# Kernel tuning notes

Hardware: AMD Instinct MI355X
Metric: run time of the kernel (lower is better)

Reference implementation:

```python
import jax, jax.numpy as jnp
import numpy as np
from jax import lax

HW = 256 * 256      # patch h*w
WINDOW = 65536
STRIDE = 32768


def _conv2d(x, w, b, stride, pad):
    y = lax.conv_general_dilated(x, w, (stride, stride), [(pad, pad), (pad, pad)],
                                 dimension_numbers=('NCHW', 'OIHW', 'NCHW'))
    return y + b[None, :, None, None]


def _fcn(x, w1, b1, w2, b2, w3, b3, w4, b4):
    x = jax.nn.relu(_conv2d(x, w1, b1, 6, 6))
    x = jax.nn.relu(_conv2d(x, w2, b2, 4, 4))
    x = jax.nn.relu(_conv2d(x, w3, b3, 2, 2))
    x = jax.nn.relu(_conv2d(x, w4, b4, 1, 1))
    return x


def _avgpool2(x):
    # torch AvgPool2d(2,2,padding=1), count_include_pad=True -> sum window / 4
    s = lax.reduce_window(x, 0.0, lax.add, (1, 1, 2, 2), (1, 1, 2, 2),
                          [(0, 0), (0, 0), (1, 1), (1, 1)])
    return s * 0.25


def _cca(x, qw, qb, kw, kb, vw, vb, gamma):
    B, C, H, W = x.shape
    q = _conv2d(x, qw, qb, 1, 0)   # (B, C//8, H, W)
    k = _conv2d(x, kw, kb, 1, 0)
    v = _conv2d(x, vw, vb, 1, 0)   # (B, C, H, W)
    # column (height-axis) energies with -inf on the diagonal (self position)
    eH = jnp.einsum('bchw,bcgw->bhwg', q, k)                     # (B,H,W,H')
    eH = jnp.where(jnp.eye(H, dtype=bool)[:, None, :], -jnp.inf, eH)
    # row (width-axis) energies
    eW = jnp.einsum('bchw,bchv->bhwv', q, k)                     # (B,H,W,W')
    att = jax.nn.softmax(jnp.concatenate([eH, eW], axis=3), axis=3)
    outH = jnp.einsum('bcgw,bhwg->bchw', v, att[..., :H])
    outW = jnp.einsum('bchv,bhwv->bchw', v, att[..., H:])
    return gamma * (outH + outW) + x


def _forward(x, f0_w1, f0_b1, f0_w2, f0_b2, f0_w3, f0_b3, f0_w4, f0_b4,
             f1_w1, f1_b1, f1_w2, f1_b2, f1_w3, f1_b3, f1_w4, f1_b4,
             qw, qb, kw, kb, vw, vb, gamma, cls_w, cls_b):
    B, nc, L = x.shape
    need = HW - L % HW                 # torch pads a full extra block when L % hw == 0
    xp = jnp.pad(x, ((0, 0), (0, 0), (0, need)))
    nw = (L + need - WINDOW) // STRIDE + 1
    idx = jnp.arange(nw)[:, None] * STRIDE + jnp.arange(WINDOW)[None, :]
    wins = xp[:, 0, :][:, idx]                      # (B, nw, WINDOW) ~ torch unfold
    # torch does a raw reshape (nw,1,h,w) -> (1,1,h*w,nw); row-major reshape matches
    c_in = wins.reshape(B, 1, HW, nw)
    c0 = _fcn(c_in, f0_w1, f0_b1, f0_w2, f0_b2, f0_w3, f0_b3, f0_w4, f0_b4)
    c1 = _fcn(_avgpool2(c_in), f1_w1, f1_b1, f1_w2, f1_b2, f1_w3, f1_b3, f1_w4, f1_b4)
    a0 = _cca(c0, qw, qb, kw, kb, vw, vb, gamma)
    a1 = _cca(c1, qw, qb, kw, kb, vw, vb, gamma)   # 'twoheadfcn' reuses cca_attn0
    feat = jnp.concatenate([a0.mean(axis=(2, 3)), a1.mean(axis=(2, 3))], axis=1)
    return feat @ cls_w.T + cls_b                   # dropout = identity at eval


def setup_inputs():
    key = jax.random.key(0)
    ks = jax.random.split(key, 32)

    def he(k, shape):
        fan_in = int(np.prod(shape[1:]))
        return (jax.random.normal(k, shape) / np.sqrt(fan_in)).astype(jnp.float32)

    inp = {'x': jax.random.uniform(ks[0], (2, 1, 4194304), dtype=jnp.float32)}
    shapes = [(64, 1, 12, 12), (128, 64, 8, 8), (256, 128, 5, 5), (128, 256, 3, 3)]
    for pre, off in (('f0', 1), ('f1', 9)):
        for i, s in enumerate(shapes):
            inp[f'{pre}_w{i+1}'] = he(ks[off + 2 * i], s)
            inp[f'{pre}_b{i+1}'] = (0.01 * jax.random.normal(ks[off + 2 * i + 1], (s[0],))).astype(jnp.float32)
    inp['qw'] = he(ks[17], (16, 128, 1, 1)); inp['qb'] = jnp.zeros((16,), jnp.float32)
    inp['kw'] = he(ks[18], (16, 128, 1, 1)); inp['kb'] = jnp.zeros((16,), jnp.float32)
    inp['vw'] = he(ks[19], (128, 128, 1, 1)); inp['vb'] = jnp.zeros((128,), jnp.float32)
    inp['gamma'] = jnp.full((1,), 0.1, jnp.float32)
    inp['cls_w'] = he(ks[20], (2, 256)); inp['cls_b'] = jnp.zeros((2,), jnp.float32)
    return inp


def reference(x, f0_w1, f0_b1, f0_w2, f0_b2, f0_w3, f0_b3, f0_w4, f0_b4,
              f1_w1, f1_b1, f1_w2, f1_b2, f1_w3, f1_b3, f1_w4, f1_b4,
              qw, qb, kw, kb, vw, vb, gamma, cls_w, cls_b):
    return _forward(x, f0_w1, f0_b1, f0_w2, f0_b2, f0_w3, f0_b3, f0_w4, f0_b4,
                    f1_w1, f1_b1, f1_w2, f1_b2, f1_w3, f1_b3, f1_w4, f1_b4,
                    qw, qb, kw, kb, vw, vb, gamma, cls_w, cls_b)
```

## Files before the change

kernel.cpp:

```cpp
#include <hip/hip_runtime.h>
#include <math.h>

#define BLK 256
static const long LX = 4194304;

typedef __bf16 bf16x8 __attribute__((ext_vector_type(8)));
typedef float  f32x4  __attribute__((ext_vector_type(4)));
typedef unsigned short u16;

__device__ __forceinline__ void bf16split(float x, u16& h, u16& l) {
    unsigned u = __float_as_uint(x);
    unsigned hr = (u + 0x7fffu + ((u >> 16) & 1u)) >> 16;
    h = (u16)hr;
    float hf = __uint_as_float(hr << 16);
    float r = x - hf;
    unsigned v = __float_as_uint(r);
    unsigned lr2 = (v + 0x7fffu + ((v >> 16) & 1u)) >> 16;
    l = (u16)lr2;
}

__device__ __forceinline__ float cin_val(const float* __restrict__ x, long xbase, int h, int w) {
    if ((unsigned)h >= 65536u || (unsigned)w >= 129u) return 0.f;
    long flat = (long)h * 129 + w;
    int n = (int)(flat >> 16);
    int q = (int)(flat & 65535);
    long pos = (long)n * 32768 + q;
    return (pos < LX) ? x[xbase + pos] : 0.f;
}

__global__ __launch_bounds__(256)
void conv1_mfma_k(const float* __restrict__ x, const u16* __restrict__ wbh,
                  const u16* __restrict__ wbl, const float* __restrict__ bias,
                  u16* __restrict__ outh, u16* __restrict__ outl) {
    const long SPT = 240306;
    __shared__ u16 ph[6400];
    __shared__ u16 pl[6400];
    const int tid = threadIdx.x;
    const int b = blockIdx.y;
    const long sp0 = (long)blockIdx.x * 128;
    const long xbase = (long)b * LX;
    const int ho_min = (int)sp0 / 22;
    const int flat_start = (ho_min * 6 - 6) * 129 - 6;
    for (int i = tid; i < 6400; i += 256) {
        int flat = flat_start + i;
        float v = 0.f;
        if (flat >= 0 && flat < 65536 * 129) {
            int n = flat >> 16, q = flat & 65535;
            long pos = (long)n * 32768 + q;
            if (pos < LX) v = x[xbase + pos];
        }
        u16 h, l; bf16split(v, h, l);
        ph[i] = h; pl[i] = l;
    }
    __syncthreads();

    const int lane = tid & 63, wid = tid >> 6;
    const int lr = lane & 15;
    const int lk = (lane >> 4) << 3;

    int off0[2]; int wlo[2], whi[2];
#pragma unroll
    for (int fm = 0; fm < 2; fm++) {
        int r = (wid << 5) + (fm << 4) + lr;
        long spl = sp0 + r; if (spl >= SPT) spl = SPT - 1;
        int sp = (int)spl;
        int ho = sp / 22;
        int wo = sp - ho * 22;
        off0[fm] = (ho * 6 - 6) * 129 + (wo * 6 - 6) - flat_start;
        wlo[fm] = (wo == 0) ? 1 : 0;
        whi[fm] = (wo == 21) ? 1 : 0;
    }

    f32x4 acc[2][4];
#pragma unroll
    for (int fn = 0; fn < 4; fn++) {
        float bv = bias[(fn << 4) + lr];
#pragma unroll
        for (int fm = 0; fm < 2; fm++) { f32x4 v = {bv, bv, bv, bv}; acc[fm][fn] = v; }
    }

    const bool zhi = (lk >= 16);
#pragma unroll
    for (int c = 0; c < 5; c++) {
        bf16x8 bH[4], bL[4];
#pragma unroll
        for (int fn = 0; fn < 4; fn++) {
            int oc = (fn << 4) + lr;
            bH[fn] = *(const bf16x8*)(wbh + oc * 160 + (c << 5) + lk);
            bL[fn] = *(const bf16x8*)(wbl + oc * 160 + (c << 5) + lk);
        }
        bf16x8 aH[2], aL[2];
#pragma unroll
        for (int fm = 0; fm < 2; fm++) {
            union { bf16x8 v; u16 u[8]; } uh, ul;
            if (c == 4 && zhi) {
#pragma unroll
                for (int jj = 0; jj < 8; jj++) { uh.u[jj] = 0; ul.u[jj] = 0; }
            } else {
                int t0 = (c << 5) + lk;
                int kh0 = t0 / 12;
                int r0 = t0 - kh0 * 12;
                int jst = 12 - r0;
                int base = off0[fm] + t0 + kh0 * 117;
#pragma unroll
                for (int jj = 0; jj < 8; jj++) {
                    int wrapped = (jj >= jst) ? 1 : 0;
                    int idx = base + jj + (wrapped ? 117 : 0);
                    int kw = r0 + jj - (wrapped ? 12 : 0);
                    int bad = (wlo[fm] & ((kw < 6) ? 1 : 0)) | (whi[fm] & ((kw > 8) ? 1 : 0));
                    u16 hv = ph[idx];
                    u16 lv = pl[idx];
                    uh.u[jj] = bad ? (u16)0 : hv;
                    ul.u[jj] = bad ? (u16)0 : lv;
                }
            }
            aH[fm] = uh.v; aL[fm] = ul.v;
        }
#pragma unroll
        for (int fm = 0; fm < 2; fm++)
#pragma unroll
            for (int fn = 0; fn < 4; fn++) {
                acc[fm][fn] = __builtin_amdgcn_mfma_f32_16x16x32_bf16(aL[fm], bH[fn], acc[fm][fn], 0, 0, 0);
                acc[fm][fn] = __builtin_amdgcn_mfma_f32_16x16x32_bf16(aH[fm], bL[fn], acc[fm][fn], 0, 0, 0);
                acc[fm][fn] = __builtin_amdgcn_mfma_f32_16x16x32_bf16(aH[fm], bH[fn], acc[fm][fn], 0, 0, 0);
            }
    }
    const int row0 = (lane >> 4) << 2;
#pragma unroll
    for (int fm = 0; fm < 2; fm++) {
#pragma unroll
        for (int q = 0; q < 4; q++) {
            long sp = sp0 + (wid << 5) + (fm << 4) + row0 + q;
            if (sp < SPT) {
                long obase = ((long)b * SPT + sp) << 6;
#pragma unroll
                for (int fn = 0; fn < 4; fn++) {
                    u16 h, l;
                    bf16split(fmaxf(acc[fm][fn][q], 0.f), h, l);
                    outh[obase + (fn << 4) + lr] = h;
                    outl[obase + (fn << 4) + lr] = l;
                }
            }
        }
    }
}

__global__ __launch_bounds__(256)
void conv1p_mfma_k(const float* __restrict__ pool, const u16* __restrict__ wbh,
                   const u16* __restrict__ wbl, const float* __restrict__ bias,
                   u16* __restrict__ outh, u16* __restrict__ outl) {
    const int SPT = 60082;
    const int HWP = 32769 * 65;
    __shared__ u16 ph[5504];
    __shared__ u16 pl[5504];
    const int tid = threadIdx.x;
    const int b = blockIdx.y;
    const long sp0 = (long)blockIdx.x * 128;
    const float* pb = pool + (long)b * HWP;
    const int ho_min = (int)sp0 / 11;
    const int fs = (ho_min * 6 - 6) * 65 - 6;
    for (int i = tid; i < 5504; i += 256) {
        int flat = fs + i;
        float v = (flat >= 0 && flat < HWP) ? pb[flat] : 0.f;
        u16 h, l; bf16split(v, h, l);
        ph[i] = h; pl[i] = l;
    }
    __syncthreads();

    const int lane = tid & 63, wid = tid >> 6;
    const int lr = lane & 15;
    const int lk = (lane >> 4) << 3;

    int off0[2]; int wlo[2], whi[2];
#pragma unroll
    for (int fm = 0; fm < 2; fm++) {
        int r = (wid << 5) + (fm << 4) + lr;
        long spl = sp0 + r; if (spl >= SPT) spl = SPT - 1;
        int sp = (int)spl;
        int ho = sp / 11;
        int wo = sp - ho * 11;
        off0[fm] = (ho - ho_min) * 390 + wo * 6;
        wlo[fm] = (wo == 0) ? 1 : 0;
        whi[fm] = (wo == 10) ? 1 : 0;
    }

    f32x4 acc[2][4];
#pragma unroll
    for (int fn = 0; fn < 4; fn++) {
        float bv = bias[(fn << 4) + lr];
#pragma unroll
        for (int fm = 0; fm < 2; fm++) { f32x4 v = {bv, bv, bv, bv}; acc[fm][fn] = v; }
    }

    const bool zhi = (lk >= 16);
#pragma unroll
    for (int c = 0; c < 5; c++) {
        bf16x8 bH[4], bL[4];
#pragma unroll
        for (int fn = 0; fn < 4; fn++) {
            int oc = (fn << 4) + lr;
            bH[fn] = *(const bf16x8*)(wbh + oc * 160 + (c << 5) + lk);
            bL[fn] = *(const bf16x8*)(wbl + oc * 160 + (c << 5) + lk);
        }
        bf16x8 aH[2], aL[2];
#pragma unroll
        for (int fm = 0; fm < 2; fm++) {
            union { bf16x8 v; u16 u[8]; } uh, ul;
            if (c == 4 && zhi) {
#pragma unroll
                for (int jj = 0; jj < 8; jj++) { uh.u[jj] = 0; ul.u[jj] = 0; }
            } else {
                int t0 = (c << 5) + lk;
                int kh0 = t0 / 12;
                int r0 = t0 - kh0 * 12;
                int jst = 12 - r0;
                int base = off0[fm] + kh0 * 65 + r0;
#pragma unroll
                for (int jj = 0; jj < 8; jj++) {
                    int wrapped = (jj >= jst) ? 1 : 0;
                    int idx = base + jj + (wrapped ? 53 : 0);
                    int kw = r0 + jj - (wrapped ? 12 : 0);
                    int bad = (wlo[fm] & ((kw < 6) ? 1 : 0)) | (whi[fm] & ((kw > 10) ? 1 : 0));
                    u16 hv = ph[idx];
                    u16 lv = pl[idx];
                    uh.u[jj] = bad ? (u16)0 : hv;
                    ul.u[jj] = bad ? (u16)0 : lv;
                }
            }
            aH[fm] = uh.v; aL[fm] = ul.v;
        }
#pragma unroll
        for (int fm = 0; fm < 2; fm++)
#pragma unroll
            for (int fn = 0; fn < 4; fn++) {
                acc[fm][fn] = __builtin_amdgcn_mfma_f32_16x16x32_bf16(aL[fm], bH[fn], acc[fm][fn], 0, 0, 0);
                acc[fm][fn] = __builtin_amdgcn_mfma_f32_16x16x32_bf16(aH[fm], bL[fn], acc[fm][fn], 0, 0, 0);
                acc[fm][fn] = __builtin_amdgcn_mfma_f32_16x16x32_bf16(aH[fm], bH[fn], acc[fm][fn], 0, 0, 0);
            }
    }
    const int row0 = (lane >> 4) << 2;
#pragma unroll
    for (int fm = 0; fm < 2; fm++) {
#pragma unroll
        for (int q = 0; q < 4; q++) {
            long sp = sp0 + (wid << 5) + (fm << 4) + row0 + q;
            if (sp < SPT) {
                long obase = ((long)b * SPT + sp) << 6;
#pragma unroll
                for (int fn = 0; fn < 4; fn++) {
                    u16 h, l;
                    bf16split(fmaxf(acc[fm][fn][q], 0.f), h, l);
                    outh[obase + (fn << 4) + lr] = h;
                    outl[obase + (fn << 4) + lr] = l;
                }
            }
        }
    }
}

__global__ __launch_bounds__(BLK)
void avgpool_synth_k(const float* __restrict__ x, float* __restrict__ out, int B) {
    const int Ho = 32769, Wo = 65;
    long total = (long)B * Ho * Wo;
    long idx = (long)blockIdx.x * BLK + threadIdx.x;
    if (idx >= total) return;
    int w2 = (int)(idx % Wo);
    long t = idx / Wo;
    int p2 = (int)(t % Ho);
    int b  = (int)(t / Ho);
    long xbase = (long)b * LX;
    float s = 0.f;
#pragma unroll
    for (int dh = 0; dh < 2; dh++)
#pragma unroll
        for (int dw = 0; dw < 2; dw++)
            s += cin_val(x, xbase, 2 * p2 - 1 + dh, 2 * w2 - 1 + dw);
    out[idx] = 0.25f * s;
}

struct RJob { const float* src; u16* dh; u16* dl; int Cout, Cin, Kk, type; long nel; };
struct RAll { RJob jobs[9]; int bstart[10]; };

__global__ __launch_bounds__(BLK)
void reorder_all_k(RAll a) {
    int bid = blockIdx.x;
    int ji = 0;
    while (ji < 8 && bid >= a.bstart[ji + 1]) ji++;
    RJob j = a.jobs[ji];
    long t = (long)(bid - a.bstart[ji]) * BLK + threadIdx.x;
    if (t >= j.nel) return;
    if (j.type == 0) {
        int tap = (int)(t % 160), oc = (int)(t / 160);
        float v = (tap < 144) ? j.src[oc * 144 + tap] : 0.f;
        u16 h, l; bf16split(v, h, l);
        j.dh[t] = h; j.dl[t] = l;
    } else {
        int kw = (int)(t % j.Kk);
        long r = t / j.Kk;
        int kh = (int)(r % j.Kk); r /= j.Kk;
        int ic = (int)(r % j.Cin);
        int oc = (int)(r / j.Cin);
        long dst = (long)oc * (j.Cin * j.Kk * j.Kk) + (long)(kh * j.Kk + kw) * j.Cin + ic;
        u16 h, l; bf16split(j.src[t], h, l);
        j.dh[dst] = h; j.dl[dst] = l;
    }
}

struct MJob {
    const u16* Ah; const u16* Al; const u16* Wh; const u16* Wl;
    const float* bias; float* out; float* part;
    int Hin, Win, Cin, cshift, Cout, K, S, P, Hout, Wout, relu, nks;
    long total; int nbx; int Ktot;
};

__global__ __launch_bounds__(256)
void mgemm2_k(MJob j0, MJob j1, int split) {
    __shared__ u16 lds[2][4][128 * 32];
    MJob j = j0;
    int bid = blockIdx.x;
    if (bid >= split) { j = j1; bid -= split; }
    const int bx = bid % j.nbx;
    int r2 = bid / j.nbx;
    const int nocb = j.Cout >> 7;
    const int ocb = (r2 % nocb) << 7;
    const int ks  = r2 / nocb;
    const int tid = threadIdx.x;
    const long spbase = (long)bx * 128;
    const int nchunk = j.Ktot >> 5;
    const int cbeg = (ks * nchunk) / j.nks;
    const int cend = ((ks + 1) * nchunk) / j.nks;

    const int sr = tid >> 1;
    const int sh = (tid & 1) << 4;
    long ssp = spbase + sr;
    const bool sval = ssp < j.total;
    long tt = sval ? ssp : 0;
    const int swo = (int)(tt % j.Wout); tt /= j.Wout;
    const int sho = (int)(tt % j.Hout);
    const int sb  = (int)(tt / j.Hout);
    const int sh0 = sho * j.S - j.P, sw0 = swo * j.S - j.P;
    const long ibase = (long)sb * j.Hin * j.Win;
    const long wbase = (long)(ocb + sr) * j.Ktot + sh;
    const int ssw = (sr >> 1) & 3;
    const int so0 = sr * 32 + ((((sh >> 3)    ) ^ ssw) << 3);
    const int so1 = sr * 32 + ((((sh >> 3) | 1) ^ ssw) << 3);

    uint4 rA0, rA1, rL0, rL1, rB0, rB1, rM0, rM1;
    auto fetch = [&](int c) {
        int p0 = c << 5;
        int khw = p0 >> j.cshift;
        int ic0 = p0 - (khw << j.cshift);
        int kh = khw / j.K, kw = khw - kh * j.K;
        int h = sh0 + kh, w = sw0 + kw;
        bool ok = sval && (unsigned)h < (unsigned)j.Hin && (unsigned)w < (unsigned)j.Win;
        uint4 z = make_uint4(0u, 0u, 0u, 0u);
        const long e = (ibase + (long)h * j.Win + w) * j.Cin + ic0 + sh;
        rA0 = ok ? *(const uint4*)(j.Ah + e)     : z;
        rA1 = ok ? *(const uint4*)(j.Ah + e + 8) : z;
        rL0 = ok ? *(const uint4*)(j.Al + e)     : z;
        rL1 = ok ? *(const uint4*)(j.Al + e + 8) : z;
        const long we = wbase + p0;
        rB0 = *(const uint4*)(j.Wh + we);
        rB1 = *(const uint4*)(j.Wh + we + 8);
        rM0 = *(const uint4*)(j.Wl + we);
        rM1 = *(const uint4*)(j.Wl + we + 8);
    };
    auto store = [&](int buf) {
        *(uint4*)&lds[buf][0][so0] = rA0; *(uint4*)&lds[buf][0][so1] = rA1;
        *(uint4*)&lds[buf][1][so0] = rL0; *(uint4*)&lds[buf][1][so1] = rL1;
        *(uint4*)&lds[buf][2][so0] = rB0; *(uint4*)&lds[buf][2][so1] = rB1;
        *(uint4*)&lds[buf][3][so0] = rM0; *(uint4*)&lds[buf][3][so1] = rM1;
    };

    const int lane = tid & 63;
    const int wid = tid >> 6;
    const int wm = (wid >> 1) << 6, wn = (wid & 1) << 6;
    const int lr = lane & 15;
    const int lko = (((lane >> 4)) ^ ((lr >> 1) & 3)) << 3;

    f32x4 acc[4][4];
    if (j.nks == 1) {
#pragma unroll
        for (int fn = 0; fn < 4; fn++) {
            float b = j.bias[ocb + wn + fn * 16 + lr];
#pragma unroll
            for (int fm = 0; fm < 4; fm++) { f32x4 v = {b, b, b, b}; acc[fm][fn] = v; }
        }
    } else {
#pragma unroll
        for (int fm = 0; fm < 4; fm++)
#pragma unroll
            for (int fn = 0; fn < 4; fn++) { f32x4 v = {0.f, 0.f, 0.f, 0.f}; acc[fm][fn] = v; }
    }

    fetch(cbeg); store(0);
    __syncthreads();

    for (int c = cbeg; c < cend; c++) {
        const int cur = (c - cbeg) & 1, nxt = cur ^ 1;
        const bool more = (c + 1 < cend);
        if (more) fetch(c + 1);
        const u16* Ahs = &lds[cur][0][0];
        const u16* Als = &lds[cur][1][0];
        const u16* Bhs = &lds[cur][2][0];
        const u16* Bls = &lds[cur][3][0];
        bf16x8 aH[4], aL[4], bH[4], bL[4];
#pragma unroll
        for (int f = 0; f < 4; f++) {
            aH[f] = *(const bf16x8*)(Ahs + (wm + f * 16 + lr) * 32 + lko);
            aL[f] = *(const bf16x8*)(Als + (wm + f * 16 + lr) * 32 + lko);
            bH[f] = *(const bf16x8*)(Bhs + (wn + f * 16 + lr) * 32 + lko);
            bL[f] = *(const bf16x8*)(Bls + (wn + f * 16 + lr) * 32 + lko);
        }
#pragma unroll
        for (int fm = 0; fm < 4; fm++)
#pragma unroll
            for (int fn = 0; fn < 4; fn++) {
                acc[fm][fn] = __builtin_amdgcn_mfma_f32_16x16x32_bf16(aL[fm], bH[fn], acc[fm][fn], 0, 0, 0);
                acc[fm][fn] = __builtin_amdgcn_mfma_f32_16x16x32_bf16(aH[fm], bL[fn], acc[fm][fn], 0, 0, 0);
                acc[fm][fn] = __builtin_amdgcn_mfma_f32_16x16x32_bf16(aH[fm], bH[fn], acc[fm][fn], 0, 0, 0);
            }
        if (more) store(nxt);
        __syncthreads();
    }

    const int row0 = (lane >> 4) << 2;
    if (j.nks == 1) {
#pragma unroll
        for (int fm = 0; fm < 4; fm++) {
#pragma unroll
            for (int q = 0; q < 4; q++) {
                long sp = spbase + wm + fm * 16 + row0 + q;
                if (sp < j.total) {
                    float* op = j.out + sp * j.Cout + ocb + wn + lr;
#pragma unroll
                    for (int fn = 0; fn < 4; fn++) {
                        float v = acc[fm][fn][q];
                        if (j.relu) v = fmaxf(v, 0.f);
                        op[fn * 16] = v;
                    }
                }
            }
        }
    } else {
        float* pb = j.part + ((long)ks * j.total) * j.Cout;
#pragma unroll
        for (int fm = 0; fm < 4; fm++) {
#pragma unroll
            for (int q = 0; q < 4; q++) {
                long sp = spbase + wm + fm * 16 + row0 + q;
                if (sp < j.total) {
                    float* op = pb + sp * j.Cout + ocb + wn + lr;
#pragma unroll
                    for (int fn = 0; fn < 4; fn++) op[fn * 16] = acc[fm][fn][q];
                }
            }
        }
    }
}

struct CJob {
    const float* part; const float* bias;
    float* outf; u16* outh; u16* outl;
    long n; int C; int nks; int relu;
};

__global__ __launch_bounds__(BLK)
void combine2m_k(CJob a, CJob b) {
    long q0 = a.n * (long)a.C / 4, q1 = b.n * (long)b.C / 4;
    long id = (long)blockIdx.x * BLK + threadIdx.x;
    CJob j; long f4;
    if (id < q0) { j = a; f4 = id * 4; }
    else if (id < q0 + q1) { j = b; f4 = (id - q0) * 4; }
    else return;
    long stride = j.n * (long)j.C;
    int cb = (int)(f4 % j.C);
    float4 s = *(const float4*)(j.bias + cb);
    for (int ss = 0; ss < j.nks; ss++) {
        float4 p = *(const float4*)(j.part + ss * stride + f4);
        s.x += p.x; s.y += p.y; s.z += p.z; s.w += p.w;
    }
    if (j.relu) {
        s.x = fmaxf(s.x, 0.f); s.y = fmaxf(s.y, 0.f);
        s.z = fmaxf(s.z, 0.f); s.w = fmaxf(s.w, 0.f);
    }
    if (j.outf) *(float4*)(j.outf + f4) = s;
    if (j.outh) {
        u16 hx, hy, hz, hw2, la, lb, lc, ld;
        bf16split(s.x, hx, la); bf16split(s.y, hy, lb);
        bf16split(s.z, hz, lc); bf16split(s.w, hw2, ld);
        *(ushort4*)(j.outh + f4) = make_ushort4(hx, hy, hz, hw2);
        *(ushort4*)(j.outl + f4) = make_ushort4(la, lb, lc, ld);
    }
}

__global__ __launch_bounds__(256)
void qk2_k(const float* __restrict__ in,
           const float* __restrict__ qw, const float* __restrict__ qb,
           const float* __restrict__ kw2, const float* __restrict__ kb2,
           float* __restrict__ outq, float* __restrict__ outk, long total) {
    const float* w    = blockIdx.y ? kw2 : qw;
    const float* bias = blockIdx.y ? kb2 : qb;
    float* out        = blockIdx.y ? outk : outq;
    __shared__ float As[64 * 132];
    __shared__ float Ws[128 * 16];
    int tid = threadIdx.x;
    long spbase = (long)blockIdx.x * 64;
    int r = tid >> 2;
    int cpart = (tid & 3) << 5;
    long sp = spbase + r;
    bool ok = sp < total;
    const float* ip = in + sp * 128 + cpart;
#pragma unroll
    for (int jj = 0; jj < 8; jj++) {
        float4 v = ok ? *(const float4*)(ip + jj * 4) : make_float4(0.f, 0.f, 0.f, 0.f);
        *(float4*)&As[r * 132 + cpart + jj * 4] = v;
    }
    for (int t = tid; t < 2048; t += 256) Ws[(t & 127) * 16 + (t >> 7)] = w[t];
    __syncthreads();
    int ocp = (tid & 3) << 2;
    float acc[4] = {bias[ocp], bias[ocp + 1], bias[ocp + 2], bias[ocp + 3]};
    for (int ic = 0; ic < 128; ic++) {
        float a = As[r * 132 + ic];
#pragma unroll
        for (int jj = 0; jj < 4; jj++) acc[jj] = fmaf(a, Ws[ic * 16 + ocp + jj], acc[jj]);
    }
    if (ok) {
#pragma unroll
        for (int jj = 0; jj < 4; jj++) out[sp * 16 + ocp + jj] = acc[jj];
    }
}

struct AJob {
    const float* q; const float* kk; const float* v;
    float* pacc; float* pm; float* pl;
    int B, H, W, nrt, ns, ntile;
};

__global__ __launch_bounds__(256)
void cca_part_k(AJob j0, AJob j1, int n0) {
    const int RT = 16, TG = 64;
    __shared__ float lbuf[8192];
    __shared__ float mlb2[32];
    float* kls    = lbuf;
    float* sc     = lbuf + 1088;
    float* scales = lbuf + 2176;
    AJob j = j0;
    int bid = blockIdx.x;
    if (bid >= n0) { j = j1; bid -= n0; }
    int rt = bid % j.nrt; int t = bid / j.nrt;
    int ksp = t % j.ns; t /= j.ns;
    int w = t % j.W; int b = t / j.W;
    const int H = j.H, W = j.W;
    const int tid = threadIdx.x;
    const int r = tid >> 4, l16 = tid & 15;
    const int h = rt * RT + r;
    const int hc = (h < H) ? h : (H - 1);
    const long colbase = (long)b * H * W + w;
    const long rowbase = ((long)b * H + hc) * W;

    float qreg[16];
    {
        const float* qp = j.q + (rowbase + w) * 16;
#pragma unroll
        for (int jj = 0; jj < 4; jj++) {
            float4 t4 = *(const float4*)(qp + 4 * jj);
            qreg[4*jj] = t4.x; qreg[4*jj+1] = t4.y; qreg[4*jj+2] = t4.z; qreg[4*jj+3] = t4.w;
        }
    }
    const int lane6 = tid & 63;
    const int wid = tid >> 6;
    const int c2 = lane6 << 1;
    float accv[16][2];
#pragma unroll
    for (int i = 0; i < 16; i++) { accv[i][0] = 0.f; accv[i][1] = 0.f; }

    float m = -INFINITY, l = 0.f;
    const int gp = l16 * 4;

    const int tbeg = (ksp * j.ntile) / j.ns;
    const int tend = ((ksp + 1) * j.ntile) / j.ns;
    for (int tt2 = tbeg; tt2 < tend; tt2++) {
        const int g0 = tt2 * TG;
        {
            int kr = tid >> 2, kc = (tid & 3) << 2;
            int gg = g0 + kr;
            float4 kv = make_float4(0.f, 0.f, 0.f, 0.f);
            if (gg < H) kv = *(const float4*)(j.kk + (colbase + (long)gg * W) * 16 + kc);
            kls[kr * 17 + kc + 0] = kv.x; kls[kr * 17 + kc + 1] = kv.y;
            kls[kr * 17 + kc + 2] = kv.z; kls[kr * 17 + kc + 3] = kv.w;
        }
        __syncthreads();
        float sloc[4];
#pragma unroll
        for (int i = 0; i < 4; i++) {
            int gg = g0 + gp + i;
            float d = 0.f;
#pragma unroll
            for (int c = 0; c < 16; c++) d = fmaf(qreg[c], kls[(gp + i) * 17 + c], d);
            sloc[i] = (gg >= H || gg == h) ? -INFINITY : d;
        }
        float tmax = fmaxf(fmaxf(sloc[0], sloc[1]), fmaxf(sloc[2], sloc[3]));
#pragma unroll
        for (int off = 1; off < 16; off <<= 1) tmax = fmaxf(tmax, __shfl_xor(tmax, off, 16));
        float mt = fmaxf(m, tmax);
        float scale = __expf(m - mt);
        float ps = 0.f;
#pragma unroll
        for (int i = 0; i < 4; i++) {
            float p = __expf(sloc[i] - mt);
            ps += p;
            sc[r * 68 + gp + i] = p;
        }
#pragma unroll
        for (int off = 1; off < 16; off <<= 1) ps += __shfl_xor(ps, off, 16);
        l = l * scale + ps;
        m = mt;
        if (l16 == 0) scales[r] = scale;
        __syncthreads();
        {
            float4 sA = *(const float4*)&scales[0];
            float4 sB = *(const float4*)&scales[4];
            float4 sC = *(const float4*)&scales[8];
            float4 sD = *(const float4*)&scales[12];
            float sarr[16] = {sA.x,sA.y,sA.z,sA.w, sB.x,sB.y,sB.z,sB.w,
                              sC.x,sC.y,sC.z,sC.w, sD.x,sD.y,sD.z,sD.w};
#pragma unroll
            for (int row = 0; row < 16; row++) {
                accv[row][0] *= sarr[row];
                accv[row][1] *= sarr[row];
            }
#pragma unroll
            for (int s = 0; s < 2; s++) {
                const int k0 = (wid << 4) + (s << 3);
                float2 v2[8];
#pragma unroll
                for (int kq = 0; kq < 8; kq++) {
                    int gg = g0 + k0 + kq;
                    if (gg >= H) gg = H - 1;
                    v2[kq] = *(const float2*)(j.v + (colbase + (long)gg * W) * 128 + c2);
                }
#pragma unroll
                for (int row = 0; row < 16; row++) {
                    float4 pA = *(const float4*)&sc[row * 68 + k0];
                    float4 pB = *(const float4*)&sc[row * 68 + k0 + 4];
                    accv[row][0] = fmaf(pA.x, v2[0].x, accv[row][0]);
                    accv[row][1] = fmaf(pA.x, v2[0].y, accv[row][1]);
                    accv[row][0] = fmaf(pA.y, v2[1].x, accv[row][0]);
                    accv[row][1] = fmaf(pA.y, v2[1].y, accv[row][1]);
                    accv[row][0] = fmaf(pA.z, v2[2].x, accv[row][0]);
                    accv[row][1] = fmaf(pA.z, v2[2].y, accv[row][1]);
                    accv[row][0] = fmaf(pA.w, v2[3].x, accv[row][0]);
                    accv[row][1] = fmaf(pA.w, v2[3].y, accv[row][1]);
                    accv[row][0] = fmaf(pB.x, v2[4].x, accv[row][0]);
                    accv[row][1] = fmaf(pB.x, v2[4].y, accv[row][1]);
                    accv[row][0] = fmaf(pB.y, v2[5].x, accv[row][0]);
                    accv[row][1] = fmaf(pB.y, v2[5].y, accv[row][1]);
                    accv[row][0] = fmaf(pB.z, v2[6].x, accv[row][0]);
                    accv[row][1] = fmaf(pB.z, v2[6].y, accv[row][1]);
                    accv[row][0] = fmaf(pB.w, v2[7].x, accv[row][0]);
                    accv[row][1] = fmaf(pB.w, v2[7].y, accv[row][1]);
                }
            }
        }
        __syncthreads();
    }
    if (ksp == 0) {
        float sw[3];
        float twmax = -INFINITY;
#pragma unroll
        for (int jj = 0; jj < 3; jj++) {
            sw[jj] = -INFINITY;
            if (jj < W) {
                const float* kp = j.kk + (rowbase + jj) * 16;
                float d = 0.f;
#pragma unroll
                for (int c = 0; c < 16; c++) d = fmaf(qreg[c], kp[c], d);
                sw[jj] = d;
                twmax = fmaxf(twmax, d);
            }
        }
        float mt = fmaxf(m, twmax);
        float scale = __expf(m - mt);
        l *= scale;
#pragma unroll
        for (int jj = 0; jj < 3; jj++) {
            if (jj < W) {
                float p = __expf(sw[jj] - mt);
                l += p;
                if (l16 == 0) sc[r * 68 + jj] = p;
            }
        }
        m = mt;
        if (l16 == 0) scales[r] = scale;
    }
    if (l16 == 0) { mlb2[2 * r] = m; mlb2[2 * r + 1] = l; }
    __syncthreads();
    if (ksp == 0) {
        float4 sA = *(const float4*)&scales[0];
        float4 sB = *(const float4*)&scales[4];
        float4 sC = *(const float4*)&scales[8];
        float4 sD = *(const float4*)&scales[12];
        float sarr[16] = {sA.x,sA.y,sA.z,sA.w, sB.x,sB.y,sB.z,sB.w,
                          sC.x,sC.y,sC.z,sC.w, sD.x,sD.y,sD.z,sD.w};
#pragma unroll
        for (int row = 0; row < 16; row++) {
            accv[row][0] *= sarr[row];
            accv[row][1] *= sarr[row];
            int hr = rt * RT + row;
            int hcr = (hr < H) ? hr : (H - 1);
            long rb = ((long)b * H + hcr) * W;
#pragma unroll
            for (int jj = 0; jj < 3; jj++) {
                if (jj < W) {
                    float p = sc[row * 68 + jj];
                    float2 vv = *(const float2*)(j.v + (rb + jj) * 128 + c2);
                    accv[row][0] = fmaf(p, vv.x, accv[row][0]);
                    accv[row][1] = fmaf(p, vv.y, accv[row][1]);
                }
            }
        }
    }
    __syncthreads();
#pragma unroll
    for (int row = 0; row < 16; row++) {
        *(float2*)&lbuf[(wid << 11) + (row << 7) + c2] = make_float2(accv[row][0], accv[row][1]);
    }
    __syncthreads();
    {
        int orow = tid >> 4, ocb = (tid & 15) << 3;
        int hr = rt * RT + orow;
        if (hr < H) {
            float4 r0 = make_float4(0.f, 0.f, 0.f, 0.f);
            float4 r1 = make_float4(0.f, 0.f, 0.f, 0.f);
#pragma unroll
            for (int wv = 0; wv < 4; wv++) {
                float4 a0 = *(const float4*)&lbuf[(wv << 11) + (orow << 7) + ocb];
                float4 a1 = *(const float4*)&lbuf[(wv << 11) + (orow << 7) + ocb + 4];
                r0.x += a0.x; r0.y += a0.y; r0.z += a0.z; r0.w += a0.w;
                r1.x += a1.x; r1.y += a1.y; r1.z += a1.z; r1.w += a1.w;
            }
            long qi = ((long)b * H + hr) * W + w;
            float* pp = j.pacc + (qi * j.ns + ksp) * 128 + ocb;
            *(float4*)pp       = r0;
            *(float4*)(pp + 4) = r1;
            if ((tid & 15) == 0) {
                j.pm[qi * j.ns + ksp] = mlb2[2 * orow];
                j.pl[qi * j.ns + ksp] = mlb2[2 * orow + 1];
            }
        }
    }
}

struct CCJob {
    const float* x; const float* pacc; const float* pm; const float* pl;
    float* out; long rows; int ns;
};

__global__ __launch_bounds__(BLK)
void cca_comb_k(CCJob a, CCJob b, const float* __restrict__ gamma) {
    long q0 = a.rows * 32, q1 = b.rows * 32;
    long id = (long)blockIdx.x * BLK + threadIdx.x;
    CCJob j; long lid;
    if (id < q0) { j = a; lid = id; }
    else if (id < q0 + q1) { j = b; lid = id - q0; }
    else return;
    long qi = lid >> 5;
    int c4 = (int)(lid & 31) << 2;
    int ns = j.ns;
    float M = -INFINITY;
    for (int s = 0; s < ns; s++) M = fmaxf(M, j.pm[qi * ns + s]);
    float L = 0.f;
    float4 acc = make_float4(0.f, 0.f, 0.f, 0.f);
    for (int s = 0; s < ns; s++) {
        float wgt = __expf(j.pm[qi * ns + s] - M);
        L += j.pl[qi * ns + s] * wgt;
        float4 p = *(const float4*)(j.pacc + (qi * ns + s) * 128 + c4);
        acc.x = fmaf(wgt, p.x, acc.x); acc.y = fmaf(wgt, p.y, acc.y);
        acc.z = fmaf(wgt, p.z, acc.z); acc.w = fmaf(wgt, p.w, acc.w);
    }
    float g = gamma[0] / L;
    float4 xr = *(const float4*)(j.x + qi * 128 + c4);
    float4 o = make_float4(g * acc.x + xr.x, g * acc.y + xr.y,
                           g * acc.z + xr.z, g * acc.w + xr.w);
    *(float4*)(j.out + qi * 128 + c4) = o;
}

__global__ __launch_bounds__(BLK)
void mean_part_k(const float* __restrict__ a, float* __restrict__ part, int HW, int NS) {
    int bx = blockIdx.x;
    int b = bx / NS, sc_ = bx % NS;
    int tid = threadIdx.x;
    int c = tid & 127, half = tid >> 7;
    int per = (HW + NS - 1) / NS;
    int s0 = sc_ * per, s1 = s0 + per; if (s1 > HW) s1 = HW;
    float acc = 0.f;
    for (int s = s0 + half; s < s1; s += 2) acc += a[((long)b * HW + s) * 128 + c];
    __shared__ float red[BLK];
    red[tid] = acc; __syncthreads();
    if (half == 0) part[(long)bx * 128 + c] = red[c] + red[c + 128];
}

__global__ __launch_bounds__(BLK)
void final2_k(const float* __restrict__ part0, const float* __restrict__ part1, int NS,
              const float* __restrict__ w, const float* __restrict__ bias,
              float* __restrict__ out, float hw0, float hw1) {
    __shared__ float feat[512];
    int tid = threadIdx.x;
    for (int t = tid; t < 512; t += BLK) {
        int b = t >> 8, c = t & 255;
        float s = 0.f;
        if (c < 128) {
            for (int ns = 0; ns < NS; ns++) s += part0[((long)b * NS + ns) * 128 + c];
            s /= hw0;
        } else {
            int cc = c - 128;
            for (int ns = 0; ns < NS; ns++) s += part1[((long)b * NS + ns) * 128 + cc];
            s /= hw1;
        }
        feat[t] = s;
    }
    __syncthreads();
    if (tid < 4) {
        int b = tid >> 1, jj = tid & 1;
        float s = bias[jj];
        for (int c = 0; c < 256; c++) s += feat[b * 256 + c] * w[jj * 256 + c];
        out[b * 2 + jj] = s;
    }
}

static inline long cdiv(long a, long b) { return (a + b - 1) / b; }

extern "C" void kernel_launch(void* const* d_in, const int* in_sizes, int n_in,
                              void* d_out, int out_size, void* d_ws, size_t ws_size,
                              hipStream_t stream) {
    const float* x     = (const float*)d_in[0];
    const float* f0w1  = (const float*)d_in[1];
    const float* f0b1  = (const float*)d_in[2];
    const float* f0w2  = (const float*)d_in[3];
    const float* f0b2  = (const float*)d_in[4];
    const float* f0w3  = (const float*)d_in[5];
    const float* f0b3  = (const float*)d_in[6];
    const float* f0w4  = (const float*)d_in[7];
    const float* f0b4  = (const float*)d_in[8];
    const float* f1w1  = (const float*)d_in[9];
    const float* f1b1  = (const float*)d_in[10];
    const float* f1w2  = (const float*)d_in[11];
    const float* f1b2  = (const float*)d_in[12];
    const float* f1w3  = (const float*)d_in[13];
    const float* f1b3  = (const float*)d_in[14];
    const float* f1w4  = (const float*)d_in[15];
    const float* f1b4  = (const float*)d_in[16];
    const float* qw    = (const float*)d_in[17];
    const float* qb    = (const float*)d_in[18];
    const float* kw    = (const float*)d_in[19];
    const float* kb    = (const float*)d_in[20];
    const float* vw    = (const float*)d_in[21];
    const float* vb    = (const float*)d_in[22];
    const float* gamma = (const float*)d_in[23];
    const float* clsw  = (const float*)d_in[24];
    const float* clsb  = (const float*)d_in[25];
    float* ws = (float*)d_ws;
    float* outp = (float*)d_out;

    const int B = 2;
    size_t off = 0;
    auto alloc = [&](size_t nfl) { size_t o = off; off += (nfl + 63) & ~(size_t)63; return o; };
    size_t o_pool = alloc((size_t)B * 32769 * 65);
    size_t o_A0h  = alloc((size_t)B * 10923 * 22 * 32);
    size_t o_A0l  = alloc((size_t)B * 10923 * 22 * 32);
    size_t o_A1h  = alloc((size_t)B * 5462 * 11 * 32);
    size_t o_A1l  = alloc((size_t)B * 5462 * 11 * 32);
    size_t o_B0h  = alloc((size_t)B * 2731 * 6 * 64);
    size_t o_B0l  = alloc((size_t)B * 2731 * 6 * 64);
    size_t o_c0   = alloc((size_t)B * 1366 * 3 * 128);
    size_t o_c1   = alloc((size_t)B * 683 * 2 * 128);
    size_t o_w1mh = alloc((size_t)64 * 160 / 2);
    size_t o_w1ml = alloc((size_t)64 * 160 / 2);
    size_t o_w1nh = alloc((size_t)64 * 160 / 2);
    size_t o_w1nl = alloc((size_t)64 * 160 / 2);
    size_t o_w2h0 = alloc((size_t)128 * 4096 / 2);
    size_t o_w2l0 = alloc((size_t)128 * 4096 / 2);
    size_t o_w2h1 = alloc((size_t)128 * 4096 / 2);
    size_t o_w2l1 = alloc((size_t)128 * 4096 / 2);
    size_t o_w3h0 = alloc((size_t)256 * 3200 / 2);
    size_t o_w3l0 = alloc((size_t)256 * 3200 / 2);
    size_t o_w3h1 = alloc((size_t)256 * 3200 / 2);
    size_t o_w3l1 = alloc((size_t)256 * 3200 / 2);
    size_t o_w4h0 = alloc((size_t)128 * 2304 / 2);
    size_t o_w4l0 = alloc((size_t)128 * 2304 / 2);
    size_t o_w4h1 = alloc((size_t)128 * 2304 / 2);
    size_t o_w4l1 = alloc((size_t)128 * 2304 / 2);
    size_t o_wvh  = alloc((size_t)128 * 128 / 2);
    size_t o_wvl  = alloc((size_t)128 * 128 / 2);
    const size_t part_small = (size_t)2 * 40968 * 128;
    const size_t part_big   = (size_t)3 * 40968 * 128;
    size_t o_part = alloc(part_big);
    size_t need_big = off;
    size_t need_small = o_part + part_small;
    size_t o_B1h = o_pool;
    size_t o_B1l = o_pool + (size_t)B * 1366 * 3 * 64;
    size_t sub = o_A0h;
    auto salloc = [&](size_t nfl) { size_t o = sub; sub += (nfl + 63) & ~(size_t)63; return o; };
    size_t o_C0h = salloc((size_t)B * 1366 * 3 * 128);
    size_t o_C0l = salloc((size_t)B * 1366 * 3 * 128);
    size_t o_C1h = salloc((size_t)B * 683 * 2 * 128);
    size_t o_C1l = salloc((size_t)B * 683 * 2 * 128);
    size_t o_c0h = salloc((size_t)B * 1366 * 3 * 64);
    size_t o_c0l = salloc((size_t)B * 1366 * 3 * 64);
    size_t o_c1h = salloc((size_t)B * 683 * 2 * 64);
    size_t o_c1l = salloc((size_t)B * 683 * 2 * 64);
    size_t o_q0  = salloc((size_t)B * 1366 * 3 * 16);
    size_t o_k0  = salloc((size_t)B * 1366 * 3 * 16);
    size_t o_v0  = salloc((size_t)B * 1366 * 3 * 128);
    size_t o_a0  = salloc((size_t)B * 1366 * 3 * 128);
    size_t o_q1  = salloc((size_t)B * 683 * 2 * 16);
    size_t o_k1  = salloc((size_t)B * 683 * 2 * 16);
    size_t o_v1  = salloc((size_t)B * 683 * 2 * 128);
    size_t o_a1  = salloc((size_t)B * 683 * 2 * 128);
    size_t o_p0  = salloc((size_t)B * 8 * 128);
    size_t o_p1  = salloc((size_t)B * 8 * 128);
    if (ws_size < need_small * sizeof(float)) {
        hipMemsetAsync(d_out, 0, (size_t)out_size * sizeof(float), stream);
        return;
    }
    const bool bigp = (ws_size >= need_big * sizeof(float));
    const int nks2 = bigp ? 3 : 2;
    const int nks3 = bigp ? 5 : 3;
    const int nks4 = bigp ? 5 : 6;
    auto U16 = [&](size_t o) { return (u16*)(ws + o); };

    {
        long tot = (long)B * 32769 * 65;
        avgpool_synth_k<<<dim3(cdiv(tot, BLK)), BLK, 0, stream>>>(x, ws + o_pool, B);
    }
    {
        RAll ra;
        auto mkR = [&](int i, const float* src, size_t dh, size_t dl,
                       int Cout, int Cin, int Kk, int type, long nel) {
            ra.jobs[i] = { src, U16(dh), U16(dl), Cout, Cin, Kk, type, nel };
        };
        mkR(0, f0w1, o_w1mh, o_w1ml, 64, 1, 12, 0, 64 * 160);
        mkR(1, f1w1, o_w1nh, o_w1nl, 64, 1, 12, 0, 64 * 160);
        mkR(2, f0w2, o_w2h0, o_w2l0, 128, 64, 8, 1, (long)128 * 64 * 64);
        mkR(3, f1w2, o_w2h1, o_w2l1, 128, 64, 8, 1, (long)128 * 64 * 64);
        mkR(4, f0w3, o_w3h0, o_w3l0, 256, 128, 5, 1, (long)256 * 128 * 25);
        mkR(5, f1w3, o_w3h1, o_w3l1, 256, 128, 5, 1, (long)256 * 128 * 25);
        mkR(6, f0w4, o_w4h0, o_w4l0, 128, 256, 3, 1, (long)128 * 256 * 9);
        mkR(7, f1w4, o_w4h1, o_w4l1, 128, 256, 3, 1, (long)128 * 256 * 9);
        mkR(8, vw,   o_wvh,  o_wvl,  128, 128, 1, 1, (long)128 * 128);
        int acc2 = 0;
        for (int i = 0; i < 9; i++) {
            ra.bstart[i] = acc2;
            acc2 += (int)cdiv(ra.jobs[i].nel, BLK);
        }
        ra.bstart[9] = acc2;
        reorder_all_k<<<dim3(acc2), BLK, 0, stream>>>(ra);
    }
    {
        int nbx = (int)cdiv(60082L, 128);
        conv1p_mfma_k<<<dim3(nbx, B), 256, 0, stream>>>(
            ws + o_pool, U16(o_w1nh), U16(o_w1nl), f1b1, U16(o_A1h), U16(o_A1l));
    }
    {
        int nbx = (int)cdiv(240306L, 128);
        conv1_mfma_k<<<dim3(nbx, B), 256, 0, stream>>>(
            x, U16(o_w1mh), U16(o_w1ml), f0b1, U16(o_A0h), U16(o_A0l));
    }

    float* partp = ws + o_part;
    auto mkM = [&](size_t ah, size_t al, size_t wh, size_t wl, const float* bias, float* out,
                   int Hin, int Win, int Cin, int cshift, int Cout,
                   int K, int S, int P, int Hout, int Wout, int relu) {
        MJob g;
        g.Ah = U16(ah); g.Al = U16(al); g.Wh = U16(wh); g.Wl = U16(wl);
        g.bias = bias; g.out = out; g.part = nullptr;
        g.Hin = Hin; g.Win = Win; g.Cin = Cin; g.cshift = cshift; g.Cout = Cout;
        g.K = K; g.S = S; g.P = P; g.Hout = Hout; g.Wout = Wout; g.relu = relu; g.nks = 1;
        g.total = (long)B * Hout * Wout;
        g.nbx = (int)((g.total + 127) / 128);
        g.Ktot = K * K * Cin;
        return g;
    };
    auto launchM = [&](MJob a, MJob b, int nks) {
        a.nks = nks; b.nks = nks;
        a.part = partp;
        b.part = partp + (size_t)nks * a.total * a.Cout;
        int na = a.nbx * (a.Cout >> 7) * nks;
        int nb = b.nbx * (b.Cout >> 7) * nks;
        mgemm2_k<<<dim3(na + nb), 256, 0, stream>>>(a, b, na);
    };

    {
        MJob a = mkM(o_A0h, o_A0l, o_w2h0, o_w2l0, f0b2, nullptr, 10923, 22, 64, 6, 128, 8, 4, 4, 2731, 6, 1);
        MJob b = mkM(o_A1h, o_A1l, o_w2h1, o_w2l1, f1b2, nullptr, 5462, 11, 64, 6, 128, 8, 4, 4, 1366, 3, 1);
        launchM(a, b, nks2);
        CJob ca = {partp, f0b2, nullptr, U16(o_B0h), U16(o_B0l), a.total, 128, nks2, 1};
        CJob cb = {partp + (size_t)nks2 * a.total * 128, f1b2, nullptr, U16(o_B1h), U16(o_B1l), b.total, 128, nks2, 1};
        long n4 = (a.total * 128 + b.total * 128) / 4;
        combine2m_k<<<dim3(cdiv(n4, BLK)), BLK, 0, stream>>>(ca, cb);
    }
    {
        MJob a = mkM(o_B0h, o_B0l, o_w3h0, o_w3l0, f0b3, nullptr, 2731, 6, 128, 7, 256, 5, 2, 2, 1366, 3, 1);
        MJob b = mkM(o_B1h, o_B1l, o_w3h1, o_w3l1, f1b3, nullptr, 1366, 3, 128, 7, 256, 5, 2, 2, 683, 2, 1);
        launchM(a, b, nks3);
        CJob ca = {partp, f0b3, nullptr, U16(o_C0h), U16(o_C0l), a.total, 256, nks3, 1};
        CJob cb = {partp + (size_t)nks3 * a.total * 256, f1b3, nullptr, U16(o_C1h), U16(o_C1l), b.total, 256, nks3, 1};
        long n4 = (a.total * 256 + b.total * 256) / 4;
        combine2m_k<<<dim3(cdiv(n4, BLK)), BLK, 0, stream>>>(ca, cb);
    }
    {
        MJob a = mkM(o_C0h, o_C0l, o_w4h0, o_w4l0, f0b4, nullptr, 1366, 3, 256, 8, 128, 3, 1, 1, 1366, 3, 1);
        MJob b = mkM(o_C1h, o_C1l, o_w4h1, o_w4l1, f1b4, nullptr, 683, 2, 256, 8, 128, 3, 1, 1, 683, 2, 1);
        launchM(a, b, nks4);
        CJob ca = {partp, f0b4, ws + o_c0, U16(o_c0h), U16(o_c0l), a.total, 128, nks4, 1};
        CJob cb = {partp + (size_t)nks4 * a.total * 128, f1b4, ws + o_c1, U16(o_c1h), U16(o_c1l), b.total, 128, nks4, 1};
        long n4 = (a.total * 128 + b.total * 128) / 4;
        combine2m_k<<<dim3(cdiv(n4, BLK)), BLK, 0, stream>>>(ca, cb);
    }
    {
        long tot0 = (long)B * 1366 * 3;
        qk2_k<<<dim3(cdiv(tot0, 64), 2), 256, 0, stream>>>(
            ws + o_c0, qw, qb, kw, kb, ws + o_q0, ws + o_k0, tot0);
        long tot1 = (long)B * 683 * 2;
        qk2_k<<<dim3(cdiv(tot1, 64), 2), 256, 0, stream>>>(
            ws + o_c1, qw, qb, kw, kb, ws + o_q1, ws + o_k1, tot1);
    }
    {
        MJob a = mkM(o_c0h, o_c0l, o_wvh, o_wvl, vb, ws + o_v0, 1366, 3, 128, 7, 128, 1, 1, 0, 1366, 3, 0);
        MJob b = mkM(o_c1h, o_c1l, o_wvh, o_wvl, vb, ws + o_v1, 683, 2, 128, 7, 128, 1, 1, 0, 683, 2, 0);
        launchM(a, b, 1);
    }
    {
        const int nrt0 = 86, nrt1 = 43;
        const int ns0 = 6, ns1 = 3;
        const long rows0 = (long)B * 1366 * 3;
        const long rows1 = (long)B * 683 * 2;
        size_t pp = o_part;
        auto palloc = [&](size_t nfl) { size_t o = pp; pp += (nfl + 63) & ~(size_t)63; return o; };
        size_t o_pa0 = palloc((size_t)rows0 * ns0 * 128);
        size_t o_pm0 = palloc((size_t)rows0 * ns0);
        size_t o_pl0 = palloc((size_t)rows0 * ns0);
        size_t o_pa1 = palloc((size_t)rows1 * ns1 * 128);
        size_t o_pm1 = palloc((size_t)rows1 * ns1);
        size_t o_pl1 = palloc((size_t)rows1 * ns1);
        AJob a0 = { ws + o_q0, ws + o_k0, ws + o_v0,
                    ws + o_pa0, ws + o_pm0, ws + o_pl0, B, 1366, 3, nrt0, ns0, 22 };
        AJob a1 = { ws + o_q1, ws + o_k1, ws + o_v1,
                    ws + o_pa1, ws + o_pm1, ws + o_pl1, B, 683, 2, nrt1, ns1, 11 };
        int n0 = B * 3 * nrt0 * ns0;
        int n1 = B * 2 * nrt1 * ns1;
        cca_part_k<<<dim3(n0 + n1), 256, 0, stream>>>(a0, a1, n0);
        CCJob c0 = { ws + o_c0, ws + o_pa0, ws + o_pm0, ws + o_pl0, ws + o_a0, rows0, ns0 };
        CCJob c1 = { ws + o_c1, ws + o_pa1, ws + o_pm1, ws + o_pl1, ws + o_a1, rows1, ns1 };
        long tot = (rows0 + rows1) * 32;
        cca_comb_k<<<dim3(cdiv(tot, BLK)), BLK, 0, stream>>>(c0, c1, gamma);
    }
    mean_part_k<<<dim3(B * 8), BLK, 0, stream>>>(ws + o_a0, ws + o_p0, 1366 * 3, 8);
    mean_part_k<<<dim3(B * 8), BLK, 0, stream>>>(ws + o_a1, ws + o_p1, 683 * 2, 8);
    final2_k<<<dim3(1), BLK, 0, stream>>>(ws + o_p0, ws + o_p1, 8, clsw, clsb, outp,
                                          (float)(1366 * 3), (float)(683 * 2));
}
```

Before: 694.7 us.

## Single-buffer weight tiles in LDS and fix split-K counts

```diff
diff --git a/kernel.cpp b/kernel.cpp
--- a/kernel.cpp
+++ b/kernel.cpp
@@ -315,7 +315,8 @@
 
 __global__ __launch_bounds__(256)
 void mgemm2_k(MJob j0, MJob j1, int split) {
-    __shared__ u16 lds[2][4][128 * 32];
+    __shared__ u16 ldsA[2][2][128 * 32];
+    __shared__ u16 ldsB[2][128 * 32];
     MJob j = j0;
     int bid = blockIdx.x;
     if (bid >= split) { j = j1; bid -= split; }
@@ -365,11 +366,13 @@
         rM0 = *(const uint4*)(j.Wl + we);
         rM1 = *(const uint4*)(j.Wl + we + 8);
     };
-    auto store = [&](int buf) {
-        *(uint4*)&lds[buf][0][so0] = rA0; *(uint4*)&lds[buf][0][so1] = rA1;
-        *(uint4*)&lds[buf][1][so0] = rL0; *(uint4*)&lds[buf][1][so1] = rL1;
-        *(uint4*)&lds[buf][2][so0] = rB0; *(uint4*)&lds[buf][2][so1] = rB1;
-        *(uint4*)&lds[buf][3][so0] = rM0; *(uint4*)&lds[buf][3][so1] = rM1;
+    auto storeA = [&](int buf) {
+        *(uint4*)&ldsA[buf][0][so0] = rA0; *(uint4*)&ldsA[buf][0][so1] = rA1;
+        *(uint4*)&ldsA[buf][1][so0] = rL0; *(uint4*)&ldsA[buf][1][so1] = rL1;
+    };
+    auto storeB = [&]() {
+        *(uint4*)&ldsB[0][so0] = rB0; *(uint4*)&ldsB[0][so1] = rB1;
+        *(uint4*)&ldsB[1][so0] = rM0; *(uint4*)&ldsB[1][so1] = rM1;
     };
 
     const int lane = tid & 63;
@@ -393,17 +396,17 @@
             for (int fn = 0; fn < 4; fn++) { f32x4 v = {0.f, 0.f, 0.f, 0.f}; acc[fm][fn] = v; }
     }
 
-    fetch(cbeg); store(0);
+    fetch(cbeg); storeA(0); storeB();
     __syncthreads();
 
     for (int c = cbeg; c < cend; c++) {
         const int cur = (c - cbeg) & 1, nxt = cur ^ 1;
         const bool more = (c + 1 < cend);
         if (more) fetch(c + 1);
-        const u16* Ahs = &lds[cur][0][0];
-        const u16* Als = &lds[cur][1][0];
-        const u16* Bhs = &lds[cur][2][0];
-        const u16* Bls = &lds[cur][3][0];
+        const u16* Ahs = &ldsA[cur][0][0];
+        const u16* Als = &ldsA[cur][1][0];
+        const u16* Bhs = &ldsB[0][0];
+        const u16* Bls = &ldsB[1][0];
         bf16x8 aH[4], aL[4], bH[4], bL[4];
 #pragma unroll
         for (int f = 0; f < 4; f++) {
@@ -412,6 +415,8 @@
             bH[f] = *(const bf16x8*)(Bhs + (wn + f * 16 + lr) * 32 + lko);
             bL[f] = *(const bf16x8*)(Bls + (wn + f * 16 + lr) * 32 + lko);
         }
+        __syncthreads();
+        if (more) { storeA(nxt); storeB(); }
 #pragma unroll
         for (int fm = 0; fm < 4; fm++)
 #pragma unroll
@@ -420,7 +425,6 @@
                 acc[fm][fn] = __builtin_amdgcn_mfma_f32_16x16x32_bf16(aH[fm], bL[fn], acc[fm][fn], 0, 0, 0);
                 acc[fm][fn] = __builtin_amdgcn_mfma_f32_16x16x32_bf16(aH[fm], bH[fn], acc[fm][fn], 0, 0, 0);
             }
-        if (more) store(nxt);
         __syncthreads();
     }
 
@@ -893,11 +897,8 @@
     size_t o_w4l1 = alloc((size_t)128 * 2304 / 2);
     size_t o_wvh  = alloc((size_t)128 * 128 / 2);
     size_t o_wvl  = alloc((size_t)128 * 128 / 2);
-    const size_t part_small = (size_t)2 * 40968 * 128;
-    const size_t part_big   = (size_t)3 * 40968 * 128;
-    size_t o_part = alloc(part_big);
-    size_t need_big = off;
-    size_t need_small = o_part + part_small;
+    size_t o_part = alloc((size_t)2 * (32772 + 8196) * 128);
+    size_t need_main = off;
     size_t o_B1h = o_pool;
     size_t o_B1l = o_pool + (size_t)B * 1366 * 3 * 64;
     size_t sub = o_A0h;
@@ -920,14 +921,10 @@
     size_t o_a1  = salloc((size_t)B * 683 * 2 * 128);
     size_t o_p0  = salloc((size_t)B * 8 * 128);
     size_t o_p1  = salloc((size_t)B * 8 * 128);
-    if (ws_size < need_small * sizeof(float)) {
+    if (ws_size < need_main * sizeof(float)) {
         hipMemsetAsync(d_out, 0, (size_t)out_size * sizeof(float), stream);
         return;
     }
-    const bool bigp = (ws_size >= need_big * sizeof(float));
-    const int nks2 = bigp ? 3 : 2;
-    const int nks3 = bigp ? 5 : 3;
-    const int nks4 = bigp ? 5 : 6;
     auto U16 = [&](size_t o) { return (u16*)(ws + o); };
 
     {
@@ -994,27 +991,27 @@
     {
         MJob a = mkM(o_A0h, o_A0l, o_w2h0, o_w2l0, f0b2, nullptr, 10923, 22, 64, 6, 128, 8, 4, 4, 2731, 6, 1);
         MJob b = mkM(o_A1h, o_A1l, o_w2h1, o_w2l1, f1b2, nullptr, 5462, 11, 64, 6, 128, 8, 4, 4, 1366, 3, 1);
-        launchM(a, b, nks2);
-        CJob ca = {partp, f0b2, nullptr, U16(o_B0h), U16(o_B0l), a.total, 128, nks2, 1};
-        CJob cb = {partp + (size_t)nks2 * a.total * 128, f1b2, nullptr, U16(o_B1h), U16(o_B1l), b.total, 128, nks2, 1};
+        launchM(a, b, 2);
+        CJob ca = {partp, f0b2, nullptr, U16(o_B0h), U16(o_B0l), a.total, 128, 2, 1};
+        CJob cb = {partp + (size_t)2 * a.total * 128, f1b2, nullptr, U16(o_B1h), U16(o_B1l), b.total, 128, 2, 1};
         long n4 = (a.total * 128 + b.total * 128) / 4;
         combine2m_k<<<dim3(cdiv(n4, BLK)), BLK, 0, stream>>>(ca, cb);
     }
     {
         MJob a = mkM(o_B0h, o_B0l, o_w3h0, o_w3l0, f0b3, nullptr, 2731, 6, 128, 7, 256, 5, 2, 2, 1366, 3, 1);
         MJob b = mkM(o_B1h, o_B1l, o_w3h1, o_w3l1, f1b3, nullptr, 1366, 3, 128, 7, 256, 5, 2, 2, 683, 2, 1);
-        launchM(a, b, nks3);
-        CJob ca = {partp, f0b3, nullptr, U16(o_C0h), U16(o_C0l), a.total, 256, nks3, 1};
-        CJob cb = {partp + (size_t)nks3 * a.total * 256, f1b3, nullptr, U16(o_C1h), U16(o_C1l), b.total, 256, nks3, 1};
+        launchM(a, b, 3);
+        CJob ca = {partp, f0b3, nullptr, U16(o_C0h), U16(o_C0l), a.total, 256, 3, 1};
+        CJob cb = {partp + (size_t)3 * a.total * 256, f1b3, nullptr, U16(o_C1h), U16(o_C1l), b.total, 256, 3, 1};
         long n4 = (a.total * 256 + b.total * 256) / 4;
         combine2m_k<<<dim3(cdiv(n4, BLK)), BLK, 0, stream>>>(ca, cb);
     }
     {
         MJob a = mkM(o_C0h, o_C0l, o_w4h0, o_w4l0, f0b4, nullptr, 1366, 3, 256, 8, 128, 3, 1, 1, 1366, 3, 1);
         MJob b = mkM(o_C1h, o_C1l, o_w4h1, o_w4l1, f1b4, nullptr, 683, 2, 256, 8, 128, 3, 1, 1, 683, 2, 1);
-        launchM(a, b, nks4);
-        CJob ca = {partp, f0b4, ws + o_c0, U16(o_c0h), U16(o_c0l), a.total, 128, nks4, 1};
-        CJob cb = {partp + (size_t)nks4 * a.total * 128, f1b4, ws + o_c1, U16(o_c1h), U16(o_c1l), b.total, 128, nks4, 1};
+        launchM(a, b, 6);
+        CJob ca = {partp, f0b4, ws + o_c0, U16(o_c0h), U16(o_c0l), a.total, 128, 6, 1};
+        CJob cb = {partp + (size_t)6 * a.total * 128, f1b4, ws + o_c1, U16(o_c1h), U16(o_c1l), b.total, 128, 6, 1};
         long n4 = (a.total * 128 + b.total * 128) / 4;
         combine2m_k<<<dim3(cdiv(n4, BLK)), BLK, 0, stream>>>(ca, cb);
     }
```

Result: slower. 734.8 us (+5.8%).
